# Kernel tuning notes

Measured on AMD Instinct MI355X. Metric: run time of the kernel, lower is better.

Reference implementation:

```python
import jax, jax.numpy as jnp
import numpy as np
from jax import lax

B, C, D, H, W = 2, 64, 16, 16, 16  # n = D*H*W = 4096; conv output length = n-2 = 4094
K = 3  # conv kernel size, dilation=2, padding=1


def setup_inputs() -> dict:
    key = jax.random.key(0)
    k1, k2, k3 = jax.random.split(key, 3)
    x = jax.random.normal(k1, (B, C, D, H, W), dtype=jnp.float32)
    # Conv1d params: weight [out_ch, in_ch, k], bias [out_ch]; PyTorch default init scale
    fan_in = C * K
    bound = 1.0 / np.sqrt(fan_in)
    conv_w = jax.random.uniform(k2, (C, C, K), jnp.float32, -bound, bound)
    conv_b = jax.random.uniform(k3, (C,), jnp.float32, -bound, bound)
    return {"x": x, "conv_w": conv_w, "conv_b": conv_b}


def _dspa(x, conv_w, conv_b):
    b, c, d, h, w = x.shape
    x1 = x.reshape(b, c, -1)  # [b, c, n]
    # dilated Conv1d: kernel=3, stride=1, padding=1, dilation=2 -> length n-2
    x2 = lax.conv_general_dilated(
        x1, conv_w,
        window_strides=(1,), padding=[(1, 1)], rhs_dilation=(2,),
        dimension_numbers=("NCH", "OIH", "NCH"),
    ) + conv_b[None, :, None]  # [b, c, n-2]
    # scores = bmm(x1^T, x2): [b, n, n-2]
    scores = jnp.einsum("bcn,bcm->bnm", x1, x2)
    # torch nn.Softmax() (dim=None) on a 3D tensor resolves to dim=0 (legacy behavior)
    x3 = jax.nn.softmax(scores, axis=0)  # [b, n, n-2]
    # x4 = bmm(x2, x3^T): [b, c, n]
    x4 = jnp.einsum("bcm,bnm->bcn", x2, x3)
    out = x1 + x4
    return out.reshape(b, c, d, h, w)


def reference(x, conv_w, conv_b):
    return _dspa(x, conv_w, conv_b)
```

## Files before the change

### kernel.cpp

```cpp
#include <hip/hip_runtime.h>

typedef unsigned short u16;
typedef unsigned int u32;
typedef __attribute__((ext_vector_type(8))) short bf16x8;
typedef __attribute__((ext_vector_type(4))) float f32x4;

#define NJ 4094

__device__ __forceinline__ u16 f2bf(float f) {
  union { float f; unsigned u; } v;
  v.f = f;
  unsigned r = v.u + 0x7fffu + ((v.u >> 16) & 1u);
  return (u16)(r >> 16);
}

__device__ __forceinline__ u32 pk_bf(float a, float b) {
  u32 ua = __float_as_uint(a) + 0x8000u;
  u32 ub = __float_as_uint(b) + 0x8000u;
  return __builtin_amdgcn_perm(ub, ua, 0x07060302u);
}

template <bool WRITE_OUT>
__global__ __launch_bounds__(256) void conv_kernel(
    const float* __restrict__ x, const float* __restrict__ w,
    const float* __restrict__ bias, u16* __restrict__ x2n, u16* __restrict__ x2T,
    u16* __restrict__ x1T, float* __restrict__ out) {
  __shared__ float xs[64 * 36];
  __shared__ float wl[64 * 64 * 3];
  const int b = blockIdx.x >> 7, jt = blockIdx.x & 127;
  const int t = threadIdx.x;
  for (int idx = t; idx < 64 * 36; idx += 256) {
    int i = idx / 36, p = idx - i * 36;
    int jg = jt * 32 - 1 + p;
    xs[idx] = (jg >= 0 && jg < 4096) ? x[(b * 64 + i) * 4096 + jg] : 0.f;
  }
  for (int idx = t; idx < 64 * 64 * 3; idx += 256) {
    int tap = idx % 3, ci = idx / 3;
    int c = ci >> 6, i = ci & 63;
    wl[(i * 64 + c) * 3 + tap] = w[idx];
  }
  __syncthreads();
  for (int idx = t; idx < 32 * 64; idx += 256) {
    int il = idx >> 6, c = idx & 63;
    float v = xs[c * 36 + il + 1];
    x1T[(b * 4096 + jt * 32 + il) * 64 + c] = f2bf(b ? -v : v);
  }
  if (WRITE_OUT) {
    for (int idx = t; idx < 64 * 32; idx += 256) {
      int i = idx >> 5, k = idx & 31;
      out[(b * 64 + i) * 4096 + jt * 32 + k] = xs[i * 36 + k + 1];
    }
  }
  const int c = t & 63, jsub = t >> 6;
  float acc[8];
  float bv = bias[c];
#pragma unroll
  for (int k = 0; k < 8; k++) acc[k] = bv;
  for (int i = 0; i < 64; i++) {
    float w0 = wl[(i * 64 + c) * 3 + 0];
    float w1 = wl[(i * 64 + c) * 3 + 1];
    float w2 = wl[(i * 64 + c) * 3 + 2];
    const float* xr = &xs[i * 36 + jsub * 8];
#pragma unroll
    for (int k = 0; k < 8; k++)
      acc[k] += w0 * xr[k] + w1 * xr[k + 2] + w2 * xr[k + 4];
  }
#pragma unroll
  for (int k = 0; k < 8; k++) {
    int jg = jt * 32 + jsub * 8 + k;
    u16 hv = f2bf(jg < NJ ? acc[k] : 0.f);
    x2n[(b * 64 + c) * 4096 + jg] = hv;
    x2T[(b * 4096 + jg) * 64 + c] = hv;
  }
}

template <bool ATOMIC>
__global__ __launch_bounds__(256, 4) void fused_kernel(
    const u16* __restrict__ x1T_g, const u16* __restrict__ x2n_g,
    const u16* __restrict__ x2T_g, u16* __restrict__ part_g,
    float* __restrict__ out) {
  __shared__ u16 P[2][2 * 64 * 72];
  const int t = threadIdx.x;
  const int wave = t >> 6, lane = t & 63;
  const int q = lane >> 4, ln = lane & 15;
  const int i0 = blockIdx.x * 64;
  const int jc = blockIdx.y;

  bf16x8 b1[2][4][2];
#pragma unroll
  for (int b = 0; b < 2; b++)
#pragma unroll
    for (int ist = 0; ist < 4; ist++)
#pragma unroll
      for (int kc = 0; kc < 2; kc++)
        b1[b][ist][kc] = *(const bf16x8*)&x1T_g[(b * 4096 + i0 + ist * 16 + ln) * 64 + kc * 32 + q * 8];

  f32x4 acc[2][4];
#pragma unroll
  for (int a = 0; a < 2; a++)
#pragma unroll
    for (int bq = 0; bq < 4; bq++) acc[a][bq] = (f32x4){0.f, 0.f, 0.f, 0.f};

  const int b2 = wave >> 1, cs2 = (wave & 1) * 2;

  for (int jt = jc * 4; jt < jc * 4 + 4; jt++) {
    const int j0 = jt * 64;
    u16* Ps = P[jt & 1];
    f32x4 ps[4];
#pragma unroll
    for (int ist = 0; ist < 4; ist++) ps[ist] = (f32x4){0.f, 0.f, 0.f, 0.f};
#pragma unroll
    for (int b = 0; b < 2; b++)
#pragma unroll
      for (int kc = 0; kc < 2; kc++) {
        bf16x8 af = *(const bf16x8*)&x2T_g[(b * 4096 + j0 + wave * 16 + ln) * 64 + kc * 32 + q * 8];
#pragma unroll
        for (int ist = 0; ist < 4; ist++)
          ps[ist] = __builtin_amdgcn_mfma_f32_16x16x32_bf16(af, b1[b][ist][kc], ps[ist], 0, 0, 0);
      }
#pragma unroll
    for (int ist = 0; ist < 4; ist++) {
      float p0[4], p1[4];
#pragma unroll
      for (int r = 0; r < 4; r++) {
        float e = __expf(-ps[ist][r]);
        p0[r] = __builtin_amdgcn_rcpf(1.f + e);
        p1[r] = 1.f - p0[r];
      }
      uint2 o0 = make_uint2(pk_bf(p0[0], p0[1]), pk_bf(p0[2], p0[3]));
      uint2 o1 = make_uint2(pk_bf(p1[0], p1[1]), pk_bf(p1[2], p1[3]));
      *(uint2*)&Ps[(0 + ist * 16 + ln) * 72 + wave * 16 + q * 4] = o0;
      *(uint2*)&Ps[(64 + ist * 16 + ln) * 72 + wave * 16 + q * 4] = o1;
    }
    __syncthreads();
#pragma unroll
    for (int kc = 0; kc < 2; kc++) {
      bf16x8 af2[2], pb[4];
#pragma unroll
      for (int cst = 0; cst < 2; cst++)
        af2[cst] = *(const bf16x8*)&x2n_g[(b2 * 64 + (cs2 + cst) * 16 + ln) * 4096 + j0 + kc * 32 + q * 8];
#pragma unroll
      for (int ist = 0; ist < 4; ist++)
        pb[ist] = *(const bf16x8*)&Ps[(b2 * 64 + ist * 16 + ln) * 72 + kc * 32 + q * 8];
#pragma unroll
      for (int cst = 0; cst < 2; cst++)
#pragma unroll
        for (int ist = 0; ist < 4; ist++)
          acc[cst][ist] =
              __builtin_amdgcn_mfma_f32_16x16x32_bf16(af2[cst], pb[ist], acc[cst][ist], 0, 0, 0);
    }
  }
  if (ATOMIC) {
#pragma unroll
    for (int cst = 0; cst < 2; cst++)
#pragma unroll
      for (int ist = 0; ist < 4; ist++)
#pragma unroll
        for (int r = 0; r < 4; r++) {
          int c = (cs2 + cst) * 16 + q * 4 + r;
          int ii = i0 + ist * 16 + ln;
          unsafeAtomicAdd(&out[(b2 * 64 + c) * 4096 + ii], acc[cst][ist][r]);
        }
  } else {
    __syncthreads();
    float* scr = (float*)P;
#pragma unroll
    for (int cst = 0; cst < 2; cst++)
#pragma unroll
      for (int ist = 0; ist < 4; ist++)
#pragma unroll
        for (int r = 0; r < 4; r++) {
          int c = (cs2 + cst) * 16 + q * 4 + r;
          scr[(b2 * 64 + c) * 68 + ist * 16 + ln] = acc[cst][ist][r];
        }
    __syncthreads();
#pragma unroll
    for (int rep = 0; rep < 4; rep++) {
      int idx = rep * 256 + t;
      int crow = idx >> 3, ck = idx & 7;
      const float* s = &scr[crow * 68 + ck * 8];
      u32 w0 = pk_bf(s[0], s[1]), w1 = pk_bf(s[2], s[3]);
      u32 w2 = pk_bf(s[4], s[5]), w3 = pk_bf(s[6], s[7]);
      int b = crow >> 6, c = crow & 63;
      u16* dst = &part_g[(size_t)((jc * 2 + b) * 64 + c) * 4096 + i0 + ck * 8];
      *(uint4*)dst = make_uint4(w0, w1, w2, w3);
    }
  }
}

__global__ __launch_bounds__(256) void reduce_kernel(
    const float* __restrict__ x, const u16* __restrict__ part,
    float* __restrict__ out) {
  int off = (blockIdx.x * 256 + threadIdx.x) * 4;
  float4 s = *(const float4*)&x[off];
#pragma unroll
  for (int j = 0; j < 16; j++) {
    uint2 pw = *(const uint2*)&part[(size_t)j * 524288 + off];
    s.x += __uint_as_float(pw.x << 16);
    s.y += __uint_as_float(pw.x & 0xffff0000u);
    s.z += __uint_as_float(pw.y << 16);
    s.w += __uint_as_float(pw.y & 0xffff0000u);
  }
  *(float4*)&out[off] = s;
}

extern "C" void kernel_launch(void* const* d_in, const int* in_sizes, int n_in,
                              void* d_out, int out_size, void* d_ws, size_t ws_size,
                              hipStream_t stream) {
  const float* x = (const float*)d_in[0];
  const float* w = (const float*)d_in[1];
  const float* bias = (const float*)d_in[2];
  float* out = (float*)d_out;
  u16* x2n = (u16*)d_ws;
  u16* x2T = x2n + 2 * 64 * 4096;
  u16* x1T = x2T + 2 * 64 * 4096;
  u16* part = x1T + 2 * 64 * 4096;

  const size_t need = 3u * (2 * 64 * 4096 * 2) + 16u * 2 * 64 * 4096 * 2;
  dim3 grid(64, 16);
  if (ws_size >= need) {
    conv_kernel<false><<<256, 256, 0, stream>>>(x, w, bias, x2n, x2T, x1T, out);
    fused_kernel<false><<<grid, 256, 0, stream>>>(x1T, x2n, x2T, part, out);
    reduce_kernel<<<512, 256, 0, stream>>>(x, part, out);
  } else {
    conv_kernel<true><<<256, 256, 0, stream>>>(x, w, bias, x2n, x2T, x1T, out);
    fused_kernel<true><<<grid, 256, 0, stream>>>(x1T, x2n, x2T, nullptr, out);
  }
}
```

Before: 110.4 us.

## Give each wave private score tile and split conv output channels across blocks

```diff
diff --git a/kernel.cpp b/kernel.cpp
--- a/kernel.cpp
+++ b/kernel.cpp
@@ -26,48 +26,51 @@
     const float* __restrict__ bias, u16* __restrict__ x2n, u16* __restrict__ x2T,
     u16* __restrict__ x1T, float* __restrict__ out) {
   __shared__ float xs[64 * 36];
-  __shared__ float wl[64 * 64 * 3];
-  const int b = blockIdx.x >> 7, jt = blockIdx.x & 127;
+  __shared__ float wl[64 * 32 * 3];
+  const int b = blockIdx.x >> 8, jt = (blockIdx.x >> 1) & 127, ch = blockIdx.x & 1;
   const int t = threadIdx.x;
   for (int idx = t; idx < 64 * 36; idx += 256) {
     int i = idx / 36, p = idx - i * 36;
     int jg = jt * 32 - 1 + p;
     xs[idx] = (jg >= 0 && jg < 4096) ? x[(b * 64 + i) * 4096 + jg] : 0.f;
   }
-  for (int idx = t; idx < 64 * 64 * 3; idx += 256) {
-    int tap = idx % 3, ci = idx / 3;
-    int c = ci >> 6, i = ci & 63;
-    wl[(i * 64 + c) * 3 + tap] = w[idx];
+  for (int idx = t; idx < 32 * 64 * 3; idx += 256) {
+    int tap = idx % 3, rest = idx / 3;
+    int co = rest >> 6, i = rest & 63;
+    wl[(i * 32 + co) * 3 + tap] = w[ch * 6144 + idx];
   }
   __syncthreads();
-  for (int idx = t; idx < 32 * 64; idx += 256) {
-    int il = idx >> 6, c = idx & 63;
-    float v = xs[c * 36 + il + 1];
-    x1T[(b * 4096 + jt * 32 + il) * 64 + c] = f2bf(b ? -v : v);
-  }
-  if (WRITE_OUT) {
-    for (int idx = t; idx < 64 * 32; idx += 256) {
-      int i = idx >> 5, k = idx & 31;
-      out[(b * 64 + i) * 4096 + jt * 32 + k] = xs[i * 36 + k + 1];
-    }
-  }
-  const int c = t & 63, jsub = t >> 6;
-  float acc[8];
+  if (ch == 0) {
+    for (int idx = t; idx < 32 * 64; idx += 256) {
+      int il = idx >> 6, c = idx & 63;
+      float v = xs[c * 36 + il + 1];
+      x1T[(b * 4096 + jt * 32 + il) * 64 + c] = f2bf(b ? -v : v);
+    }
+    if (WRITE_OUT) {
+      for (int idx = t; idx < 64 * 32; idx += 256) {
+        int i = idx >> 5, k = idx & 31;
+        out[(b * 64 + i) * 4096 + jt * 32 + k] = xs[i * 36 + k + 1];
+      }
+    }
+  }
+  const int co = t & 31, jsub = t >> 5;
+  const int c = ch * 32 + co;
+  float acc[4];
   float bv = bias[c];
 #pragma unroll
-  for (int k = 0; k < 8; k++) acc[k] = bv;
+  for (int k = 0; k < 4; k++) acc[k] = bv;
   for (int i = 0; i < 64; i++) {
-    float w0 = wl[(i * 64 + c) * 3 + 0];
-    float w1 = wl[(i * 64 + c) * 3 + 1];
-    float w2 = wl[(i * 64 + c) * 3 + 2];
-    const float* xr = &xs[i * 36 + jsub * 8];
-#pragma unroll
-    for (int k = 0; k < 8; k++)
+    float w0 = wl[(i * 32 + co) * 3 + 0];
+    float w1 = wl[(i * 32 + co) * 3 + 1];
+    float w2 = wl[(i * 32 + co) * 3 + 2];
+    const float* xr = &xs[i * 36 + jsub * 4];
+#pragma unroll
+    for (int k = 0; k < 4; k++)
       acc[k] += w0 * xr[k] + w1 * xr[k + 2] + w2 * xr[k + 4];
   }
 #pragma unroll
-  for (int k = 0; k < 8; k++) {
-    int jg = jt * 32 + jsub * 8 + k;
+  for (int k = 0; k < 4; k++) {
+    int jg = jt * 32 + jsub * 4 + k;
     u16 hv = f2bf(jg < NJ ? acc[k] : 0.f);
     x2n[(b * 64 + c) * 4096 + jg] = hv;
     x2T[(b * 4096 + jg) * 64 + c] = hv;
@@ -79,111 +82,102 @@
     const u16* __restrict__ x1T_g, const u16* __restrict__ x2n_g,
     const u16* __restrict__ x2T_g, u16* __restrict__ part_g,
     float* __restrict__ out) {
-  __shared__ u16 P[2][2 * 64 * 72];
+  __shared__ __align__(16) char smem[18432];
   const int t = threadIdx.x;
   const int wave = t >> 6, lane = t & 63;
   const int q = lane >> 4, ln = lane & 15;
   const int i0 = blockIdx.x * 64;
+  const int iw = i0 + wave * 16;
   const int jc = blockIdx.y;
-
-  bf16x8 b1[2][4][2];
+  u16* Pw = (u16*)(smem + wave * 4608);
+
+  bf16x8 b1[2][2];
 #pragma unroll
   for (int b = 0; b < 2; b++)
 #pragma unroll
-    for (int ist = 0; ist < 4; ist++)
-#pragma unroll
-      for (int kc = 0; kc < 2; kc++)
-        b1[b][ist][kc] = *(const bf16x8*)&x1T_g[(b * 4096 + i0 + ist * 16 + ln) * 64 + kc * 32 + q * 8];
+    for (int kc = 0; kc < 2; kc++)
+      b1[b][kc] = *(const bf16x8*)&x1T_g[(b * 4096 + iw + ln) * 64 + kc * 32 + q * 8];
 
   f32x4 acc[2][4];
 #pragma unroll
   for (int a = 0; a < 2; a++)
 #pragma unroll
     for (int bq = 0; bq < 4; bq++) acc[a][bq] = (f32x4){0.f, 0.f, 0.f, 0.f};
-
-  const int b2 = wave >> 1, cs2 = (wave & 1) * 2;
 
   for (int jt = jc * 4; jt < jc * 4 + 4; jt++) {
     const int j0 = jt * 64;
-    u16* Ps = P[jt & 1];
     f32x4 ps[4];
 #pragma unroll
-    for (int ist = 0; ist < 4; ist++) ps[ist] = (f32x4){0.f, 0.f, 0.f, 0.f};
+    for (int js = 0; js < 4; js++) ps[js] = (f32x4){0.f, 0.f, 0.f, 0.f};
 #pragma unroll
     for (int b = 0; b < 2; b++)
 #pragma unroll
-      for (int kc = 0; kc < 2; kc++) {
-        bf16x8 af = *(const bf16x8*)&x2T_g[(b * 4096 + j0 + wave * 16 + ln) * 64 + kc * 32 + q * 8];
-#pragma unroll
-        for (int ist = 0; ist < 4; ist++)
-          ps[ist] = __builtin_amdgcn_mfma_f32_16x16x32_bf16(af, b1[b][ist][kc], ps[ist], 0, 0, 0);
-      }
-#pragma unroll
-    for (int ist = 0; ist < 4; ist++) {
+      for (int kc = 0; kc < 2; kc++)
+#pragma unroll
+        for (int js = 0; js < 4; js++) {
+          bf16x8 af = *(const bf16x8*)&x2T_g[(b * 4096 + j0 + js * 16 + ln) * 64 + kc * 32 + q * 8];
+          ps[js] = __builtin_amdgcn_mfma_f32_16x16x32_bf16(af, b1[b][kc], ps[js], 0, 0, 0);
+        }
+#pragma unroll
+    for (int js = 0; js < 4; js++) {
       float p0[4], p1[4];
 #pragma unroll
       for (int r = 0; r < 4; r++) {
-        float e = __expf(-ps[ist][r]);
+        float e = __expf(-ps[js][r]);
         p0[r] = __builtin_amdgcn_rcpf(1.f + e);
         p1[r] = 1.f - p0[r];
       }
       uint2 o0 = make_uint2(pk_bf(p0[0], p0[1]), pk_bf(p0[2], p0[3]));
       uint2 o1 = make_uint2(pk_bf(p1[0], p1[1]), pk_bf(p1[2], p1[3]));
-      *(uint2*)&Ps[(0 + ist * 16 + ln) * 72 + wave * 16 + q * 4] = o0;
-      *(uint2*)&Ps[(64 + ist * 16 + ln) * 72 + wave * 16 + q * 4] = o1;
-    }
-    __syncthreads();
+      *(uint2*)&Pw[(0 + ln) * 72 + js * 16 + q * 4] = o0;
+      *(uint2*)&Pw[(16 + ln) * 72 + js * 16 + q * 4] = o1;
+    }
 #pragma unroll
     for (int kc = 0; kc < 2; kc++) {
-      bf16x8 af2[2], pb[4];
-#pragma unroll
-      for (int cst = 0; cst < 2; cst++)
-        af2[cst] = *(const bf16x8*)&x2n_g[(b2 * 64 + (cs2 + cst) * 16 + ln) * 4096 + j0 + kc * 32 + q * 8];
-#pragma unroll
-      for (int ist = 0; ist < 4; ist++)
-        pb[ist] = *(const bf16x8*)&Ps[(b2 * 64 + ist * 16 + ln) * 72 + kc * 32 + q * 8];
-#pragma unroll
-      for (int cst = 0; cst < 2; cst++)
-#pragma unroll
-        for (int ist = 0; ist < 4; ist++)
-          acc[cst][ist] =
-              __builtin_amdgcn_mfma_f32_16x16x32_bf16(af2[cst], pb[ist], acc[cst][ist], 0, 0, 0);
+      bf16x8 pb[2];
+#pragma unroll
+      for (int b = 0; b < 2; b++)
+        pb[b] = *(const bf16x8*)&Pw[(b * 16 + ln) * 72 + kc * 32 + q * 8];
+#pragma unroll
+      for (int b = 0; b < 2; b++)
+#pragma unroll
+        for (int cst = 0; cst < 4; cst++) {
+          bf16x8 af2 = *(const bf16x8*)&x2n_g[(b * 64 + cst * 16 + ln) * 4096 + j0 + kc * 32 + q * 8];
+          acc[b][cst] = __builtin_amdgcn_mfma_f32_16x16x32_bf16(af2, pb[b], acc[b][cst], 0, 0, 0);
+        }
     }
   }
   if (ATOMIC) {
 #pragma unroll
-    for (int cst = 0; cst < 2; cst++)
-#pragma unroll
-      for (int ist = 0; ist < 4; ist++)
+    for (int b = 0; b < 2; b++)
+#pragma unroll
+      for (int cst = 0; cst < 4; cst++)
 #pragma unroll
         for (int r = 0; r < 4; r++) {
-          int c = (cs2 + cst) * 16 + q * 4 + r;
-          int ii = i0 + ist * 16 + ln;
-          unsafeAtomicAdd(&out[(b2 * 64 + c) * 4096 + ii], acc[cst][ist][r]);
+          int c = cst * 16 + q * 4 + r;
+          unsafeAtomicAdd(&out[(b * 64 + c) * 4096 + iw + ln], acc[b][cst][r]);
         }
   } else {
-    __syncthreads();
-    float* scr = (float*)P;
-#pragma unroll
-    for (int cst = 0; cst < 2; cst++)
-#pragma unroll
-      for (int ist = 0; ist < 4; ist++)
-#pragma unroll
-        for (int r = 0; r < 4; r++) {
-          int c = (cs2 + cst) * 16 + q * 4 + r;
-          scr[(b2 * 64 + c) * 68 + ist * 16 + ln] = acc[cst][ist][r];
-        }
-    __syncthreads();
-#pragma unroll
-    for (int rep = 0; rep < 4; rep++) {
-      int idx = rep * 256 + t;
-      int crow = idx >> 3, ck = idx & 7;
-      const float* s = &scr[crow * 68 + ck * 8];
-      u32 w0 = pk_bf(s[0], s[1]), w1 = pk_bf(s[2], s[3]);
-      u32 w2 = pk_bf(s[4], s[5]), w3 = pk_bf(s[6], s[7]);
-      int b = crow >> 6, c = crow & 63;
-      u16* dst = &part_g[(size_t)((jc * 2 + b) * 64 + c) * 4096 + i0 + ck * 8];
-      *(uint4*)dst = make_uint4(w0, w1, w2, w3);
+    float* scr = (float*)smem;
+#pragma unroll
+    for (int b = 0; b < 2; b++) {
+      __syncthreads();
+#pragma unroll
+      for (int cst = 0; cst < 4; cst++)
+#pragma unroll
+        for (int r = 0; r < 4; r++)
+          scr[(cst * 16 + q * 4 + r) * 68 + wave * 16 + ln] = acc[b][cst][r];
+      __syncthreads();
+#pragma unroll
+      for (int rep = 0; rep < 2; rep++) {
+        int idx = rep * 256 + t;
+        int crow = idx >> 3, ck = idx & 7;
+        const float* s = &scr[crow * 68 + ck * 8];
+        u32 w0 = pk_bf(s[0], s[1]), w1 = pk_bf(s[2], s[3]);
+        u32 w2 = pk_bf(s[4], s[5]), w3 = pk_bf(s[6], s[7]);
+        u16* dst = &part_g[(size_t)((jc * 2 + b) * 64 + crow) * 4096 + i0 + ck * 8];
+        *(uint4*)dst = make_uint4(w0, w1, w2, w3);
+      }
     }
   }
 }
@@ -219,11 +213,11 @@
   const size_t need = 3u * (2 * 64 * 4096 * 2) + 16u * 2 * 64 * 4096 * 2;
   dim3 grid(64, 16);
   if (ws_size >= need) {
-    conv_kernel<false><<<256, 256, 0, stream>>>(x, w, bias, x2n, x2T, x1T, out);
+    conv_kernel<false><<<512, 256, 0, stream>>>(x, w, bias, x2n, x2T, x1T, out);
     fused_kernel<false><<<grid, 256, 0, stream>>>(x1T, x2n, x2T, part, out);
     reduce_kernel<<<512, 256, 0, stream>>>(x, part, out);
   } else {
-    conv_kernel<true><<<256, 256, 0, stream>>>(x, w, bias, x2n, x2T, x1T, out);
+    conv_kernel<true><<<512, 256, 0, stream>>>(x, w, bias, x2n, x2T, x1T, out);
     fused_kernel<true><<<grid, 256, 0, stream>>>(x1T, x2n, x2T, nullptr, out);
   }
 }
```

Measured after the change: 140.9 us. 1.28x slower.
